# Kernel optimization log

Hardware: AMD Instinct MI355X
Metric: run time of the kernel (lower is better)

Reference implementation:

```python
import jax, jax.numpy as jnp
import numpy as np

NUM_LEVELS = 4
RADIUS = 4


def _avg_pool2(x):
    # x: [N, H, W] -> [N, H//2, W//2], 2x2 mean pool, stride 2 (F.avg_pool2d(corr,2,2))
    N, H, W = x.shape
    return x.reshape(N, H // 2, 2, W // 2, 2).mean(axis=(2, 4))


def _bilinear_sample(img, x, y):
    # img: [N, H, W]; x, y: [N, P] pixel coords.
    # Matches F.grid_sample(..., mode='bilinear', align_corners=True, padding_mode='zeros')
    # after the pixel->normalized->pixel round trip in bilinear_sampler (identity).
    N, H, W = img.shape
    x0 = jnp.floor(x)
    y0 = jnp.floor(y)
    wx = x - x0
    wy = y - y0
    x0i = x0.astype(jnp.int32)
    y0i = y0.astype(jnp.int32)
    flat = img.reshape(N, H * W)

    def gather(yi, xi):
        valid = (xi >= 0) & (xi <= W - 1) & (yi >= 0) & (yi <= H - 1)
        idx = jnp.clip(yi, 0, H - 1) * W + jnp.clip(xi, 0, W - 1)
        v = jnp.take_along_axis(flat, idx, axis=1)
        return jnp.where(valid, v, jnp.zeros((), img.dtype))

    v00 = gather(y0i, x0i)
    v01 = gather(y0i, x0i + 1)
    v10 = gather(y0i + 1, x0i)
    v11 = gather(y0i + 1, x0i + 1)
    return (v00 * (1 - wy) * (1 - wx) + v01 * (1 - wy) * wx
            + v10 * wy * (1 - wx) + v11 * wy * wx)


def _corr_block(fmap1, fmap2, coords):
    B, D, H, W = fmap1.shape
    # all-pairs correlation: [B, H*W, H*W] / sqrt(D)
    f1 = fmap1.reshape(B, D, H * W)
    f2 = fmap2.reshape(B, D, H * W)
    corr = jnp.einsum('bdn,bdm->bnm', f1, f2) / jnp.sqrt(jnp.asarray(D, fmap1.dtype))
    corr = corr.reshape(B * H * W, H, W)
    pyramid = [corr]
    for _ in range(NUM_LEVELS - 1):
        corr = _avg_pool2(corr)
        pyramid.append(corr)

    # coords: [B, 2, H, W] (x, y) -> [B*H*W, 2]
    c = coords.transpose(0, 2, 3, 1).reshape(B * H * W, 2)
    r = RADIUS
    d = jnp.linspace(-r, r, 2 * r + 1)
    dyg, dxg = jnp.meshgrid(d, d, indexing='ij')
    # faithful to torch: delta = stack(meshgrid(dy, dx), -1); channel 0 added to x, 1 to y
    delta = jnp.stack([dyg, dxg], axis=-1).reshape(-1, 2)  # [81, 2]

    outs = []
    for i, lvl in enumerate(pyramid):
        cl = c[:, None, :] / (2.0 ** i) + delta[None, :, :]  # [N, 81, 2]
        s = _bilinear_sample(lvl, cl[..., 0], cl[..., 1])    # [N, 81]
        outs.append(s.reshape(B, H, W, (2 * r + 1) ** 2))
    out = jnp.concatenate(outs, axis=-1)                     # [B, H, W, 4*81]
    return out.transpose(0, 3, 1, 2).astype(jnp.float32)


def setup_inputs() -> dict:
    key = jax.random.key(0)
    k1, k2, k3 = jax.random.split(key, 3)
    B, D, H, W = 2, 256, 80, 80
    fmap1 = jax.random.normal(k1, (B, D, H, W), dtype=jnp.float32)
    fmap2 = jax.random.normal(k2, (B, D, H, W), dtype=jnp.float32)
    # pixel coords in [0, W-1] x [0, H-1] (channel 0 = x, channel 1 = y)
    u = jax.random.uniform(k3, (B, 2, H, W), dtype=jnp.float32)
    scale = jnp.asarray([W - 1, H - 1], jnp.float32).reshape(1, 2, 1, 1)
    coords = u * scale
    return {"fmap1": fmap1, "fmap2": fmap2, "coords": coords}


def reference(fmap1, fmap2, coords):
    return _corr_block(fmap1, fmap2, coords)
```

## Files before the change

kernel.cpp:

```cpp
#include <hip/hip_runtime.h>


typedef _Float16 h2 __attribute__((ext_vector_type(2)));
typedef _Float16 half8 __attribute__((ext_vector_type(8)));
typedef float f32x4 __attribute__((ext_vector_type(4)));

#define HWDIM 80
#define DCH 256
#define NPIX 12800
#define NBUCKET 800

__global__ __launch_bounds__(256) void zero_k(float4* __restrict__ dst) {
    int i = blockIdx.x * 256 + threadIdx.x;
    dst[i] = make_float4(0.f, 0.f, 0.f, 0.f);
}

__global__ __launch_bounds__(256) void transpose_all(const float* __restrict__ f1,
                                                     const float* __restrict__ f2,
                                                     _Float16* __restrict__ f1h,
                                                     _Float16* __restrict__ f2p0) {
    __shared__ float tile[256][33];
    int bid = blockIdx.x;
    bool isf1 = bid < 400;
    int lb = isf1 ? bid : bid - 400;
    const float* src = isf1 ? f1 : f2;
    int b = lb / 200;
    int s0 = (lb % 200) * 32;
    int t = threadIdx.x;
    const float* sb = src + (size_t)b * DCH * (HWDIM * HWDIM);
#pragma unroll 4
    for (int k = 0; k < 32; ++k) {
        int j = t + 256 * k;
        int c = j >> 5, s = j & 31;
        tile[c][s] = sb[(size_t)c * (HWDIM * HWDIM) + s0 + s];
    }
    __syncthreads();
    int p = t & 127;
    int srow = t >> 7;
    if (isf1) {
        _Float16* db = f1h + ((size_t)b * 6400 + s0) * DCH;
#pragma unroll 4
        for (int k = 0; k < 16; ++k) {
            int s = 2 * k + srow;
            h2 v;
            v[0] = (_Float16)tile[2 * p][s];
            v[1] = (_Float16)tile[2 * p + 1][s];
            *(h2*)(db + (size_t)s * DCH + 2 * p) = v;
        }
    } else {
#pragma unroll 4
        for (int k = 0; k < 16; ++k) {
            int s = 2 * k + srow;
            int spatial = s0 + s;
            int yy = spatial / 80;
            int xx = spatial - yy * 80;
            h2 v;
            v[0] = (_Float16)tile[2 * p][s];
            v[1] = (_Float16)tile[2 * p + 1][s];
            size_t off = (size_t)b * 2073600 + (size_t)(p >> 4) * 259200
                       + ((size_t)(yy + 5) * 90 + (xx + 5)) * 32 + ((2 * p) & 31);
            *(h2*)(f2p0 + off) = v;
        }
    }
}

__global__ __launch_bounds__(256) void pools(const _Float16* __restrict__ l0,
                                             _Float16* __restrict__ l1,
                                             _Float16* __restrict__ l2,
                                             _Float16* __restrict__ l3) {
    int i = blockIdx.x * 256 + threadIdx.x;
    if (i < 409600) {
        int c2 = i & 15;
        int r = i >> 4;
        int x = r % 40; r /= 40;
        int y = r % 40; r /= 40;
        int pl = r & 7;
        int b = r >> 3;
        const h2* s = (const h2*)l0 + (size_t)b * 1036800 + (size_t)pl * 129600
                    + ((size_t)(2 * y + 5) * 90 + (2 * x + 5)) * 16 + c2;
        h2 v00 = s[0], v01 = s[16], v10 = s[90 * 16], v11 = s[90 * 16 + 16];
        float r0 = ((float)v00[0] + (float)v01[0] + (float)v10[0] + (float)v11[0]) * 0.25f;
        float r1 = ((float)v00[1] + (float)v01[1] + (float)v10[1] + (float)v11[1]) * 0.25f;
        h2 o; o[0] = (_Float16)r0; o[1] = (_Float16)r1;
        *((h2*)l1 + (size_t)b * 320000 + (size_t)pl * 40000
          + ((size_t)(y + 5) * 50 + (x + 5)) * 16 + c2) = o;
    } else if (i < 512000) {
        int j = i - 409600;
        int c2 = j & 15;
        int r = j >> 4;
        int x = r % 20; r /= 20;
        int y = r % 20; r /= 20;
        int pl = r & 7;
        int b = r >> 3;
        const h2* s = (const h2*)l0 + (size_t)b * 1036800 + (size_t)pl * 129600 + c2;
        float r0 = 0.f, r1 = 0.f;
#pragma unroll
        for (int dy = 0; dy < 4; ++dy)
#pragma unroll
            for (int dx = 0; dx < 4; ++dx) {
                h2 v = s[((size_t)(4 * y + dy + 5) * 90 + (4 * x + dx + 5)) * 16];
                r0 += (float)v[0];
                r1 += (float)v[1];
            }
        h2 o; o[0] = (_Float16)(r0 * 0.0625f); o[1] = (_Float16)(r1 * 0.0625f);
        *((h2*)l2 + (size_t)b * 115200 + (size_t)pl * 14400
          + ((size_t)(y + 5) * 30 + (x + 5)) * 16 + c2) = o;
    } else {
        int j = i - 512000;
        int c2 = j & 15;
        int r = j >> 4;
        int x = r % 10; r /= 10;
        int y = r % 10; r /= 10;
        int pl = r & 7;
        int b = r >> 3;
        const h2* s = (const h2*)l0 + (size_t)b * 1036800 + (size_t)pl * 129600 + c2;
        float r0 = 0.f, r1 = 0.f;
#pragma unroll
        for (int dy = 0; dy < 8; ++dy)
#pragma unroll
            for (int dx = 0; dx < 8; ++dx) {
                h2 v = s[((size_t)(8 * y + dy + 5) * 90 + (8 * x + dx + 5)) * 16];
                r0 += (float)v[0];
                r1 += (float)v[1];
            }
        h2 o; o[0] = (_Float16)(r0 * 0.015625f); o[1] = (_Float16)(r1 * 0.015625f);
        *((h2*)l3 + (size_t)b * 51200 + (size_t)pl * 6400
          + ((size_t)(y + 5) * 20 + (x + 5)) * 16 + c2) = o;
    }
}

static __device__ __forceinline__ int bucket_of(const float* coords, int n) {
    int b = n / 6400;
    int r = n - b * 6400;
    float cx = coords[(size_t)b * 12800 + r];
    float cy = coords[(size_t)b * 12800 + 6400 + r];
    int ix = min(max((int)floorf(cx), 0), 79);
    int iy = min(max((int)floorf(cy), 0), 79);
    return b * 400 + (iy >> 2) * 20 + (ix >> 2);
}

__global__ __launch_bounds__(1024) void bucket_k(const float* __restrict__ coords,
                                                 int* __restrict__ sortedIdxP,
                                                 int* __restrict__ rank) {
    __shared__ unsigned int histS[NBUCKET], startS[NBUCKET], curS[NBUCKET];
    __shared__ unsigned int waveSum[16];
    __shared__ unsigned int totalS;
    int t = threadIdx.x;
    if (t < NBUCKET) histS[t] = 0u;
    __syncthreads();
    int bkt[13];
#pragma unroll
    for (int i = 0; i < 13; ++i) {
        int n = i * 1024 + t;
        if (n < NPIX) {
            bkt[i] = bucket_of(coords, n);
            atomicAdd(&histS[bkt[i]], 1u);
        }
    }
    __syncthreads();
    unsigned int v = (t < NBUCKET) ? ((histS[t] + 15u) & ~15u) : 0u;
    unsigned int x = v;
#pragma unroll
    for (int d = 1; d < 64; d <<= 1) {
        unsigned int y = __shfl_up(x, d);
        if ((t & 63) >= d) x += y;
    }
    if ((t & 63) == 63) waveSum[t >> 6] = x;
    __syncthreads();
    if (t < 16) {
        unsigned int w = waveSum[t];
#pragma unroll
        for (int d = 1; d < 16; d <<= 1) {
            unsigned int y = __shfl_up(w, d);
            if (t >= d) w += y;
        }
        waveSum[t] = w;
    }
    __syncthreads();
    unsigned int incl = x + ((t >> 6) ? waveSum[(t >> 6) - 1] : 0u);
    if (t < NBUCKET) {
        unsigned int e = incl - v;
        startS[t] = e;
        curS[t] = e;
        if (t == NBUCKET - 1) totalS = incl;
    }
    __syncthreads();
#pragma unroll
    for (int i = 0; i < 13; ++i) {
        int n = i * 1024 + t;
        if (n < NPIX) {
            unsigned int pos = atomicAdd(&curS[bkt[i]], 1u);
            sortedIdxP[pos] = n;
            rank[n] = (int)pos;
        }
    }
    __syncthreads();
    if (t < NBUCKET) {
        unsigned int h = histS[t];
        if (h) {
            unsigned int pc = (h + 15u) & ~15u;
            unsigned int base = startS[t];
            int dup = sortedIdxP[base];
            for (unsigned int s = h; s < pc; ++s) sortedIdxP[base + s] = dup;
        }
    }
    for (unsigned int s = totalS + t; s < 25600u; s += 1024u) sortedIdxP[s] = -1;
}

template <int TB, int TE>
static __device__ __forceinline__ void run_tiles(
    int lane, int b,
    const _Float16* __restrict__ f2p0, const _Float16* __restrict__ f2p1,
    const _Float16* __restrict__ f2p2, const _Float16* __restrict__ f2p3,
    const int* X0cS, const int* Y0cS, const half8* bf, _Float16* G) {
#pragma unroll
    for (int tt = TB; tt < TE; ++tt) {
        const int L  = tt < 11 ? 0 : tt < 19 ? 1 : tt < 26 ? 2 : 3;
        const int rt = tt - (L == 0 ? 0 : L == 1 ? 11 : L == 2 ? 19 : 26);
        const int Ww = L == 0 ? 13 : L == 1 ? 11 : 10;
        const int MT = L == 0 ? 169 : L == 1 ? 121 : 100;
        const int MAG = L == 0 ? 161320 : L == 1 ? 190652 : 209716;
        const int Wp = L == 0 ? 90 : L == 1 ? 50 : L == 2 ? 30 : 20;
        const int PS = L == 0 ? 259200 : L == 1 ? 80000 : L == 2 ? 28800 : 12800;
        const int PB = L == 0 ? 2073600 : L == 1 ? 640000 : L == 2 ? 230400 : 102400;
        const int GO = L == 0 ? 0 : L == 1 ? 176 : L == 2 ? 304 : 416;
        const _Float16* f2L = (L == 0 ? f2p0 : L == 1 ? f2p1 : L == 2 ? f2p2 : f2p3);
        const _Float16* f2b = f2L + (size_t)b * PB
                            + ((size_t)(Y0cS[L] + 5) * Wp + (X0cS[L] + 5)) * 32;
        int m = min(rt * 16 + (lane & 15), MT - 1);
        int my = (m * MAG) >> 21;
        int mx = m - my * Ww;
        const float4* ap = (const float4*)(f2b + (size_t)(my * Wp + mx) * 32)
                         + (lane >> 4);
        half8 av[8];
#pragma unroll
        for (int kk = 0; kk < 8; ++kk)
            av[kk] = __builtin_bit_cast(half8, ap[kk * (PS / 8)]);
        __builtin_amdgcn_sched_barrier(0);
        f32x4 acc0 = {0.f, 0.f, 0.f, 0.f};
        f32x4 acc1 = {0.f, 0.f, 0.f, 0.f};
#pragma unroll
        for (int kk = 0; kk < 8; kk += 2) {
            acc0 = __builtin_amdgcn_mfma_f32_16x16x32_f16(av[kk], bf[kk], acc0, 0, 0, 0);
            acc1 = __builtin_amdgcn_mfma_f32_16x16x32_f16(av[kk + 1], bf[kk + 1], acc1, 0, 0, 0);
        }
        int gr = GO + rt * 16 + (lane >> 4) * 4;
#pragma unroll
        for (int r = 0; r < 4; ++r)
            G[(gr + r) * 17 + (lane & 15)] = (_Float16)(acc0[r] + acc1[r]);
    }
}

__global__ __launch_bounds__(512, 4) void corr_mfma(
    const _Float16* __restrict__ f1h,
    const _Float16* __restrict__ f2p0, const _Float16* __restrict__ f2p1,
    const _Float16* __restrict__ f2p2, const _Float16* __restrict__ f2p3,
    const float* __restrict__ coords, const int* __restrict__ sortedIdxP,
    _Float16* __restrict__ scratch) {
    __shared__ _Float16 G[528 * 17];
    __shared__ _Float16 f1S[16 * 264];
    __shared__ float fxS[4][16], fyS[4][16];
    __shared__ int lxS[4][16], lyS[4][16];
    __shared__ int X0cS[4], Y0cS[4], bS;

    int pphys = blockIdx.x;
    int l = (pphys & 7) * 200 + (pphys >> 3);
    int tid = threadIdx.x;
    if (sortedIdxP[l * 16] < 0) return;
    int lane = tid & 63;
    int wave = tid >> 6;

    {
        int px = tid >> 5, q = tid & 31;
        int n = sortedIdxP[l * 16 + px];
        const float4* src = (const float4*)(f1h + (size_t)n * DCH);
        *((float4*)(f1S + px * 264) + q) = src[q];
    }
    if (tid < 64) {
        int px = tid & 15, Lt = tid >> 4;
        int n = sortedIdxP[l * 16 + px];
        int b = n / 6400;
        int r = n - b * 6400;
        float cx = coords[(size_t)b * 12800 + r];
        float cy = coords[(size_t)b * 12800 + 6400 + r];
        float ls = 1.0f / (float)(1 << Lt);
        float cxl = cx * ls, cyl = cy * ls;
        float fxf = floorf(cxl), fyf = floorf(cyl);
        int X0 = (int)fxf - 4, Y0 = (int)fyf - 4;
        int ix = min(max((int)floorf(cx), 0), 79);
        int iy = min(max((int)floorf(cy), 0), 79);
        int X0c = (((ix >> 2) * 4) >> Lt) - 4;
        int Y0c = (((iy >> 2) * 4) >> Lt) - 4;
        lxS[Lt][px] = min(max(X0 - X0c, 0), 3);
        lyS[Lt][px] = min(max(Y0 - Y0c, 0), 3);
        fxS[Lt][px] = cxl - fxf;
        fyS[Lt][px] = cyl - fyf;
        X0cS[Lt] = X0c;
        Y0cS[Lt] = Y0c;
        if (tid == 0) bS = sortedIdxP[l * 16] / 6400;
    }
    __syncthreads();
    int b = bS;

    half8 bf[8];
#pragma unroll
    for (int kk = 0; kk < 8; ++kk)
        bf[kk] = *(const half8*)(f1S + (lane & 15) * 264 + ((lane >> 4) + 4 * kk) * 8);

    if      (wave == 0) run_tiles<0, 5>(lane, b, f2p0, f2p1, f2p2, f2p3, X0cS, Y0cS, bf, G);
    else if (wave == 1) run_tiles<5, 9>(lane, b, f2p0, f2p1, f2p2, f2p3, X0cS, Y0cS, bf, G);
    else if (wave == 2) run_tiles<9, 13>(lane, b, f2p0, f2p1, f2p2, f2p3, X0cS, Y0cS, bf, G);
    else if (wave == 3) run_tiles<13, 17>(lane, b, f2p0, f2p1, f2p2, f2p3, X0cS, Y0cS, bf, G);
    else if (wave == 4) run_tiles<17, 21>(lane, b, f2p0, f2p1, f2p2, f2p3, X0cS, Y0cS, bf, G);
    else if (wave == 5) run_tiles<21, 25>(lane, b, f2p0, f2p1, f2p2, f2p3, X0cS, Y0cS, bf, G);
    else if (wave == 6) run_tiles<25, 29>(lane, b, f2p0, f2p1, f2p2, f2p3, X0cS, Y0cS, bf, G);
    else                run_tiles<29, 33>(lane, b, f2p0, f2p1, f2p2, f2p3, X0cS, Y0cS, bf, G);
    __syncthreads();

    _Float16* sc = scratch + (size_t)l * 5184;
    for (int idx = tid; idx < 5184; idx += 512) {
        int k2 = idx >> 4, x = idx & 15;
        int Le = (k2 * 810) >> 16;
        int k = k2 - Le * 81;
        int Ww = Le == 0 ? 13 : Le == 1 ? 11 : 10;
        int GO = Le == 0 ? 0 : Le == 1 ? 176 : Le == 2 ? 304 : 416;
        int a = (k * 57) >> 9;
        int c = k - 9 * a;
        int gx = lxS[Le][x] + a, gy = lyS[Le][x] + c;
        int m00 = GO + gy * Ww + gx;
        float fx = fxS[Le][x], fy = fyS[Le][x];
        float t00 = (float)G[m00 * 17 + x];
        float t01 = (float)G[(m00 + 1) * 17 + x];
        float t10 = (float)G[(m00 + Ww) * 17 + x];
        float t11 = (float)G[(m00 + Ww + 1) * 17 + x];
        float v = ((1.f - fy) * ((1.f - fx) * t00 + fx * t01)
                 + fy * ((1.f - fx) * t10 + fx * t11)) * 0.0625f;
        sc[idx] = (_Float16)v;
    }
}

__global__ __launch_bounds__(256) void unsort4(const _Float16* __restrict__ scratch,
                                               const int* __restrict__ rank,
                                               float* __restrict__ out) {
    int u = blockIdx.x * 256 + threadIdx.x;
    int q = u % 1600;
    int ch = (u / 1600) % 324;
    int b = u / (1600 * 324);
    int nl = q * 4;
    int4 rk = *(const int4*)(rank + b * 6400 + nl);
    float4 v;
    v.x = (float)scratch[(size_t)(rk.x >> 4) * 5184 + ch * 16 + (rk.x & 15)];
    v.y = (float)scratch[(size_t)(rk.y >> 4) * 5184 + ch * 16 + (rk.y & 15)];
    v.z = (float)scratch[(size_t)(rk.z >> 4) * 5184 + ch * 16 + (rk.z & 15)];
    v.w = (float)scratch[(size_t)(rk.w >> 4) * 5184 + ch * 16 + (rk.w & 15)];
    *(float4*)(out + ((size_t)b * 324 + ch) * 6400 + nl) = v;
}

extern "C" void kernel_launch(void* const* d_in, const int* in_sizes, int n_in,
                              void* d_out, int out_size, void* d_ws, size_t ws_size,
                              hipStream_t stream) {
    const float* fmap1 = (const float*)d_in[0];
    const float* fmap2 = (const float*)d_in[1];
    const float* coords = (const float*)d_in[2];
    float* out = (float*)d_out;
    char* ws = (char*)d_ws;

    _Float16* f1h  = (_Float16*)(ws);
    _Float16* f2p0 = (_Float16*)(ws + 6553600);
    _Float16* f2p1 = (_Float16*)(ws + 14848000);
    _Float16* f2p2 = (_Float16*)(ws + 17408000);
    _Float16* f2p3 = (_Float16*)(ws + 18329600);
    int* sortedIdxP = (int*)(ws + 18739200);
    int* rank       = (int*)(ws + 18841600);
    _Float16* scratch = (_Float16*)(ws + 18892800);

    zero_k<<<dim3(2975), dim3(256), 0, stream>>>((float4*)f2p0);

    transpose_all<<<dim3(800), dim3(256), 0, stream>>>(fmap1, fmap2, f1h, f2p0);
    pools<<<dim3(2100), dim3(256), 0, stream>>>(f2p0, f2p1, f2p2, f2p3);
    bucket_k<<<dim3(1), dim3(1024), 0, stream>>>(coords, sortedIdxP, rank);
    corr_mfma<<<dim3(1600), dim3(512), 0, stream>>>(f1h, f2p0, f2p1, f2p2, f2p3,
                                                    coords, sortedIdxP, scratch);
    unsort4<<<dim3(4050), dim3(256), 0, stream>>>(scratch, rank, out);
}
```

Before: 93.75 us.

## Double corr_mfma block size and transpose scratch layout for coalesced unsort

The correlation kernel now runs 1024 threads (16 waves) per block, with each wave handling about two G tiles instead of four, to spread the MFMA work more finely. The scratch buffer is switched to a pixel-major layout padded to 352 channels. The unsort kernel is replaced by an LDS-tiled transpose that reads each pixel's contiguous channel row and writes coalesced output. This aims to remove the scattered 2-byte gathers of the old unsort. The cost is fewer unsort blocks (200) and possible register pressure or occupancy limits from the 1024-thread launch bound.

```diff
diff --git a/kernel.cpp b/kernel.cpp
--- a/kernel.cpp
+++ b/kernel.cpp
@@ -9,6 +9,7 @@
 #define DCH 256
 #define NPIX 12800
 #define NBUCKET 800
+#define CHP 352
 
 __global__ __launch_bounds__(256) void zero_k(float4* __restrict__ dst) {
     int i = blockIdx.x * 256 + threadIdx.x;
@@ -251,7 +252,7 @@
     }
 }
 
-__global__ __launch_bounds__(512, 4) void corr_mfma(
+__global__ __launch_bounds__(1024, 2) void corr_mfma(
     const _Float16* __restrict__ f1h,
     const _Float16* __restrict__ f2p0, const _Float16* __restrict__ f2p1,
     const _Float16* __restrict__ f2p2, const _Float16* __restrict__ f2p3,
@@ -270,7 +271,7 @@
     int lane = tid & 63;
     int wave = tid >> 6;
 
-    {
+    if (tid < 512) {
         int px = tid >> 5, q = tid & 31;
         int n = sortedIdxP[l * 16 + px];
         const float4* src = (const float4*)(f1h + (size_t)n * DCH);
@@ -307,18 +308,28 @@
     for (int kk = 0; kk < 8; ++kk)
         bf[kk] = *(const half8*)(f1S + (lane & 15) * 264 + ((lane >> 4) + 4 * kk) * 8);
 
-    if      (wave == 0) run_tiles<0, 5>(lane, b, f2p0, f2p1, f2p2, f2p3, X0cS, Y0cS, bf, G);
-    else if (wave == 1) run_tiles<5, 9>(lane, b, f2p0, f2p1, f2p2, f2p3, X0cS, Y0cS, bf, G);
-    else if (wave == 2) run_tiles<9, 13>(lane, b, f2p0, f2p1, f2p2, f2p3, X0cS, Y0cS, bf, G);
-    else if (wave == 3) run_tiles<13, 17>(lane, b, f2p0, f2p1, f2p2, f2p3, X0cS, Y0cS, bf, G);
-    else if (wave == 4) run_tiles<17, 21>(lane, b, f2p0, f2p1, f2p2, f2p3, X0cS, Y0cS, bf, G);
-    else if (wave == 5) run_tiles<21, 25>(lane, b, f2p0, f2p1, f2p2, f2p3, X0cS, Y0cS, bf, G);
-    else if (wave == 6) run_tiles<25, 29>(lane, b, f2p0, f2p1, f2p2, f2p3, X0cS, Y0cS, bf, G);
-    else                run_tiles<29, 33>(lane, b, f2p0, f2p1, f2p2, f2p3, X0cS, Y0cS, bf, G);
-    __syncthreads();
-
-    _Float16* sc = scratch + (size_t)l * 5184;
-    for (int idx = tid; idx < 5184; idx += 512) {
+    switch (wave) {
+    case 0:  run_tiles<0, 2>(lane, b, f2p0, f2p1, f2p2, f2p3, X0cS, Y0cS, bf, G); break;
+    case 1:  run_tiles<2, 4>(lane, b, f2p0, f2p1, f2p2, f2p3, X0cS, Y0cS, bf, G); break;
+    case 2:  run_tiles<4, 6>(lane, b, f2p0, f2p1, f2p2, f2p3, X0cS, Y0cS, bf, G); break;
+    case 3:  run_tiles<6, 8>(lane, b, f2p0, f2p1, f2p2, f2p3, X0cS, Y0cS, bf, G); break;
+    case 4:  run_tiles<8, 10>(lane, b, f2p0, f2p1, f2p2, f2p3, X0cS, Y0cS, bf, G); break;
+    case 5:  run_tiles<10, 12>(lane, b, f2p0, f2p1, f2p2, f2p3, X0cS, Y0cS, bf, G); break;
+    case 6:  run_tiles<12, 14>(lane, b, f2p0, f2p1, f2p2, f2p3, X0cS, Y0cS, bf, G); break;
+    case 7:  run_tiles<14, 16>(lane, b, f2p0, f2p1, f2p2, f2p3, X0cS, Y0cS, bf, G); break;
+    case 8:  run_tiles<16, 18>(lane, b, f2p0, f2p1, f2p2, f2p3, X0cS, Y0cS, bf, G); break;
+    case 9:  run_tiles<18, 20>(lane, b, f2p0, f2p1, f2p2, f2p3, X0cS, Y0cS, bf, G); break;
+    case 10: run_tiles<20, 22>(lane, b, f2p0, f2p1, f2p2, f2p3, X0cS, Y0cS, bf, G); break;
+    case 11: run_tiles<22, 24>(lane, b, f2p0, f2p1, f2p2, f2p3, X0cS, Y0cS, bf, G); break;
+    case 12: run_tiles<24, 26>(lane, b, f2p0, f2p1, f2p2, f2p3, X0cS, Y0cS, bf, G); break;
+    case 13: run_tiles<26, 28>(lane, b, f2p0, f2p1, f2p2, f2p3, X0cS, Y0cS, bf, G); break;
+    case 14: run_tiles<28, 30>(lane, b, f2p0, f2p1, f2p2, f2p3, X0cS, Y0cS, bf, G); break;
+    default: run_tiles<30, 33>(lane, b, f2p0, f2p1, f2p2, f2p3, X0cS, Y0cS, bf, G); break;
+    }
+    __syncthreads();
+
+    _Float16* sc = scratch + (size_t)l * 16 * CHP;
+    for (int idx = tid; idx < 5184; idx += 1024) {
         int k2 = idx >> 4, x = idx & 15;
         int Le = (k2 * 810) >> 16;
         int k = k2 - Le * 81;
@@ -335,25 +346,37 @@
         float t11 = (float)G[(m00 + Ww + 1) * 17 + x];
         float v = ((1.f - fy) * ((1.f - fx) * t00 + fx * t01)
                  + fy * ((1.f - fx) * t10 + fx * t11)) * 0.0625f;
-        sc[idx] = (_Float16)v;
-    }
-}
-
-__global__ __launch_bounds__(256) void unsort4(const _Float16* __restrict__ scratch,
-                                               const int* __restrict__ rank,
-                                               float* __restrict__ out) {
-    int u = blockIdx.x * 256 + threadIdx.x;
-    int q = u % 1600;
-    int ch = (u / 1600) % 324;
-    int b = u / (1600 * 324);
-    int nl = q * 4;
-    int4 rk = *(const int4*)(rank + b * 6400 + nl);
-    float4 v;
-    v.x = (float)scratch[(size_t)(rk.x >> 4) * 5184 + ch * 16 + (rk.x & 15)];
-    v.y = (float)scratch[(size_t)(rk.y >> 4) * 5184 + ch * 16 + (rk.y & 15)];
-    v.z = (float)scratch[(size_t)(rk.z >> 4) * 5184 + ch * 16 + (rk.z & 15)];
-    v.w = (float)scratch[(size_t)(rk.w >> 4) * 5184 + ch * 16 + (rk.w & 15)];
-    *(float4*)(out + ((size_t)b * 324 + ch) * 6400 + nl) = v;
+        sc[x * CHP + k2] = (_Float16)v;
+    }
+}
+
+__global__ __launch_bounds__(256) void unsort_t(const _Float16* __restrict__ scratch,
+                                                const int* __restrict__ rank,
+                                                float* __restrict__ out) {
+    __shared__ _Float16 lds[64][40];
+    int blk = blockIdx.x;
+    int b = blk / 100;
+    int nl0 = (blk % 100) * 64;
+    int t = threadIdx.x;
+    int p = t >> 2, j = t & 3;
+    int n = blk * 64 + p;
+    int rk = rank[n];
+    const float4* src = (const float4*)(scratch + ((size_t)(rk >> 4) * 16 + (rk & 15)) * CHP);
+    int px = t & 63, iq = t >> 6;
+
+    for (int c = 0; c < 11; ++c) {
+        float4 f4 = src[c * 4 + j];
+        *(float4*)(&lds[p][j * 8]) = f4;
+        __syncthreads();
+#pragma unroll
+        for (int w = 0; w < 8; ++w) {
+            int i = w * 4 + iq;
+            int ch = c * 32 + i;
+            if (ch < 324)
+                out[((size_t)b * 324 + ch) * 6400 + nl0 + px] = (float)lds[px][i];
+        }
+        __syncthreads();
+    }
 }
 
 extern "C" void kernel_launch(void* const* d_in, const int* in_sizes, int n_in,
@@ -379,7 +402,7 @@
     transpose_all<<<dim3(800), dim3(256), 0, stream>>>(fmap1, fmap2, f1h, f2p0);
     pools<<<dim3(2100), dim3(256), 0, stream>>>(f2p0, f2p1, f2p2, f2p3);
     bucket_k<<<dim3(1), dim3(1024), 0, stream>>>(coords, sortedIdxP, rank);
-    corr_mfma<<<dim3(1600), dim3(512), 0, stream>>>(f1h, f2p0, f2p1, f2p2, f2p3,
-                                                    coords, sortedIdxP, scratch);
-    unsort4<<<dim3(4050), dim3(256), 0, stream>>>(scratch, rank, out);
-}
+    corr_mfma<<<dim3(1600), dim3(1024), 0, stream>>>(f1h, f2p0, f2p1, f2p2, f2p3,
+                                                     coords, sortedIdxP, scratch);
+    unsort_t<<<dim3(200), dim3(256), 0, stream>>>(scratch, rank, out);
+}
```

Result: slower. 107.8 us (+15.0%).
